# Kernel optimization log

Hardware: AMD Instinct MI355X
Metric: run time of the kernel (lower is better)

Reference implementation:

```python
import jax, jax.numpy as jnp
import numpy as np

B, T, N_IN, UNITS = 256, 1000, 128, 512
TAU, THR, DT = 20.0, 0.01, 1.0
N_REFR = 0
TAU_ADAPT, BETA = 200.0, 1.6
DAMP = 0.3
ADD_CUR = 0.0


def setup_inputs() -> dict:
    key = jax.random.key(0)
    k1, k2, k3 = jax.random.split(key, 3)
    x = jax.random.normal(k1, (B, T, N_IN), jnp.float32)
    # glorot-like scaling so membrane potentials stay in a sane range
    W_in = jax.random.normal(k2, (N_IN, UNITS), jnp.float32) * (1.0 / np.sqrt(N_IN))
    W_rec = jax.random.normal(k3, (UNITS, UNITS), jnp.float32) * (1.0 / np.sqrt(UNITS))
    return {"x": x, "W_in": W_in, "W_rec": W_rec}


@jax.custom_vjp
def spike(v_scaled):
    # Heaviside spike with pseudo-derivative (dampened triangular surrogate)
    return (v_scaled > 0.0).astype(v_scaled.dtype)


def _spike_fwd(v_scaled):
    return (v_scaled > 0.0).astype(v_scaled.dtype), v_scaled


def _spike_bwd(v_scaled, g):
    return (g * DAMP * jnp.maximum(1.0 - jnp.abs(v_scaled), 0.0),)


spike.defvjp(_spike_fwd, _spike_bwd)


def alif_forward(x, W_in, W_rec):
    decay = jnp.exp(-DT / TAU)          # membrane decay
    decay_b = jnp.exp(-DT / TAU_ADAPT)  # adaptation decay
    # recurrent self-connections are disconnected (diagonal zeroed in build)
    W_rec = W_rec * (1.0 - jnp.eye(UNITS, dtype=W_rec.dtype))
    # precompute input currents for all timesteps: [T, B, UNITS]
    i_in_seq = jnp.einsum('bti,iu->tbu', x, W_in)

    def step(state, i_in):
        v, z, b, r = state
        new_b = decay_b * b + (1.0 - decay_b) * z
        thr = THR + new_b * BETA  # adaptive threshold
        i_t = i_in + z @ W_rec + ADD_CUR
        I_reset = z * thr * DT
        new_v = decay * v + (1.0 - decay) * i_t - I_reset
        z_new = spike((new_v - thr) / thr) * (1.0 / DT)
        new_z = jnp.where(r > 0.1, jnp.zeros_like(z_new), z_new)
        new_r = jnp.clip(r + N_REFR * new_z - 1.0, 0.0, float(N_REFR))
        return (new_v, new_z, new_b, new_r), new_z

    zeros = jnp.zeros((B, UNITS), jnp.float32)
    _, zs = jax.lax.scan(step, (zeros, zeros, zeros, zeros), i_in_seq)
    return jnp.transpose(zs, (1, 0, 2))  # [B, T, UNITS]


def reference(x, W_in, W_rec):
    return alif_forward(x, W_in, W_rec)
```

## Files before the change

kernel.cpp:

```cpp
#include <hip/hip_runtime.h>

#define B_SZ   256
#define T_SZ   1000
#define N_IN   128
#define UNITS  512

__global__ __launch_bounds__(512) void wz_prep(const float* __restrict__ Wr,
                                               float* __restrict__ Wz) {
    const int c = threadIdx.x, r = blockIdx.x;
    Wz[(size_t)r * UNITS + c] =
        (r >= UNITS || r == c) ? 0.0f : Wr[(size_t)r * UNITS + c];
}

__global__ __launch_bounds__(256) void gemm_in(const float* __restrict__ X,
                                               const float* __restrict__ W,
                                               float* __restrict__ C) {
    __shared__ __align__(16) float As[32][128];
    __shared__ __align__(16) float Bs[32][128];

    const int tid = threadIdx.x;
    const int ntile = blockIdx.x & 3;
    const int mtile = blockIdx.x >> 2;
    const int m0 = mtile * 128, n0 = ntile * 128;
    const int tm  = (tid >> 4) * 8;
    const int tn4 = (tid & 15) * 4;

    float acc[8][8];
#pragma unroll
    for (int i = 0; i < 8; ++i)
#pragma unroll
        for (int j = 0; j < 8; ++j) acc[i][j] = 0.0f;

    for (int k0 = 0; k0 < 128; k0 += 32) {
        __syncthreads();
#pragma unroll
        for (int r = 0; r < 4; ++r) {
            int li  = r * 256 + tid;
            int row = li >> 3;
            int ch  = li & 7;
            float4 a = *(const float4*)&X[(size_t)(m0 + row) * 128 + k0 + ch * 4];
            As[ch * 4 + 0][row] = a.x;
            As[ch * 4 + 1][row] = a.y;
            As[ch * 4 + 2][row] = a.z;
            As[ch * 4 + 3][row] = a.w;
        }
#pragma unroll
        for (int r = 0; r < 4; ++r) {
            int li = r * 256 + tid;
            int kk = li >> 5;
            int n4 = li & 31;
            *(float4*)&Bs[kk][n4 * 4] =
                *(const float4*)&W[(size_t)(k0 + kk) * 512 + n0 + n4 * 4];
        }
        __syncthreads();

#pragma unroll 8
        for (int k = 0; k < 32; ++k) {
            float4 a0 = *(const float4*)&As[k][tm];
            float4 a1 = *(const float4*)&As[k][tm + 4];
            float4 b0 = *(const float4*)&Bs[k][tn4];
            float4 b1 = *(const float4*)&Bs[k][tn4 + 64];
            const float av[8] = {a0.x, a0.y, a0.z, a0.w, a1.x, a1.y, a1.z, a1.w};
            const float bv[8] = {b0.x, b0.y, b0.z, b0.w, b1.x, b1.y, b1.z, b1.w};
#pragma unroll
            for (int i = 0; i < 8; ++i)
#pragma unroll
                for (int j = 0; j < 8; ++j)
                    acc[i][j] = fmaf(av[i], bv[j], acc[i][j]);
        }
    }

#pragma unroll
    for (int i = 0; i < 8; ++i) {
        size_t row = (size_t)(m0 + tm + i) * 512;
        float4 c0 = make_float4(acc[i][0], acc[i][1], acc[i][2], acc[i][3]);
        float4 c1 = make_float4(acc[i][4], acc[i][5], acc[i][6], acc[i][7]);
        *(float4*)&C[row + n0 + tn4]      = c0;
        *(float4*)&C[row + n0 + 64 + tn4] = c1;
    }
}

__global__ __launch_bounds__(1024, 1) void alif_scan(const float* __restrict__ Wz,
                                                     float* __restrict__ IO) {
    const int tid  = threadIdx.x;
    const int half = tid >> 9;
    const int u    = tid & 511;
    const int w    = u >> 6;
    const int lane = tid & 63;
    const int b    = blockIdx.x * 2 + half;

    __shared__ __align__(16) int s_list[2][520];
    __shared__ int s_cnt[2][8];
    __shared__ int s_total[2];

    const float DECAY   = 0.95122942450071400910f;
    const float OMD     = 1.0f - DECAY;
    const float DECAY_B = 0.99501247919268232342f;
    const float OMDB    = 1.0f - DECAY_B;

    float v = 0.0f, ad = 0.0f, z = 0.0f;

    const float* wz = Wz + u;
    float* io = IO + (size_t)b * (T_SZ * UNITS) + u;
    int* lst = s_list[half];

    lst[u] = UNITS;
    if (u < 8) lst[UNITS + u] = UNITS;
    if (u == 0) s_total[half] = 0;
    __syncthreads();

    float i_cur = io[0];

    for (int t = 0; t < T_SZ; ++t) {
        float i_next = io[(t + 1 < T_SZ ? t + 1 : t) * UNITS];

        const int cnt = s_total[half];
        float acc = 0.0f;

        for (int k = 0; k < cnt; k += 8) {
            int4 Ja = *(const int4*)(lst + k);
            int4 Jb = *(const int4*)(lst + k + 4);
            float g0 = wz[Ja.x * UNITS];
            float g1 = wz[Ja.y * UNITS];
            float g2 = wz[Ja.z * UNITS];
            float g3 = wz[Ja.w * UNITS];
            float g4 = wz[Jb.x * UNITS];
            float g5 = wz[Jb.y * UNITS];
            float g6 = wz[Jb.z * UNITS];
            float g7 = wz[Jb.w * UNITS];
            acc = __fadd_rn(acc, g0);
            acc = __fadd_rn(acc, g1);
            acc = __fadd_rn(acc, g2);
            acc = __fadd_rn(acc, g3);
            acc = __fadd_rn(acc, g4);
            acc = __fadd_rn(acc, g5);
            acc = __fadd_rn(acc, g6);
            acc = __fadd_rn(acc, g7);
        }

        float newb = __fadd_rn(__fmul_rn(DECAY_B, ad), __fmul_rn(OMDB, z));
        float thr  = __fadd_rn(0.01f, __fmul_rn(newb, 1.6f));
        float it   = __fadd_rn(__fadd_rn(i_cur, acc), 0.0f);
        float ires = __fmul_rn(__fmul_rn(z, thr), 1.0f);
        float newv = __fsub_rn(
            __fadd_rn(__fmul_rn(DECAY, v), __fmul_rn(OMD, it)), ires);
        float zn = (newv > thr) ? 1.0f : 0.0f;

        io[t * UNITS] = zn;
        v = newv; ad = newb; z = zn; i_cur = i_next;

        unsigned long long m = __ballot(zn > 0.0f);
        if (lane == 0) s_cnt[half][w] = __popcll(m);
        __syncthreads();

        int base = 0, total = 0;
#pragma unroll
        for (int i = 0; i < 8; ++i) {
            int c = s_cnt[half][i];
            total += c;
            if (i < w) base += c;
        }
        if (zn > 0.0f) {
            int pos = base + __popcll(m & ((1ull << lane) - 1ull));
            lst[pos] = u;
        }
        if (u == 0) s_total[half] = total;
        if (u < 8) lst[total + u] = UNITS;
        __syncthreads();
    }
}

extern "C" void kernel_launch(void* const* d_in, const int* in_sizes, int n_in,
                              void* d_out, int out_size, void* d_ws, size_t ws_size,
                              hipStream_t stream) {
    (void)in_sizes; (void)n_in; (void)out_size; (void)ws_size;
    const float* x     = (const float*)d_in[0];
    const float* W_in  = (const float*)d_in[1];
    const float* W_rec = (const float*)d_in[2];
    float* out = (float*)d_out;
    float* Wz  = (float*)d_ws;

    wz_prep<<<dim3(UNITS + 1), dim3(UNITS), 0, stream>>>(W_rec, Wz);
    gemm_in<<<dim3((B_SZ * T_SZ / 128) * (UNITS / 128)), dim3(256), 0, stream>>>(
        x, W_in, out);
    alif_scan<<<dim3(B_SZ / 2), dim3(1024), 0, stream>>>(Wz, out);
}
```

Measured before the change: 2.206 ms.

## Cache first recurrent weight rows in LDS and run one batch per block

```diff
diff --git a/kernel.cpp b/kernel.cpp
--- a/kernel.cpp
+++ b/kernel.cpp
@@ -4,6 +4,10 @@
 #define T_SZ   1000
 #define N_IN   128
 #define UNITS  512
+#define NC     64
+
+#define SMEM_WORDS (33280 + 528 + 8 + 4)
+#define SMEM_BYTES (SMEM_WORDS * 4)
 
 __global__ __launch_bounds__(512) void wz_prep(const float* __restrict__ Wr,
                                                float* __restrict__ Wz) {
@@ -80,18 +84,18 @@
     }
 }
 
-__global__ __launch_bounds__(1024, 1) void alif_scan(const float* __restrict__ Wz,
-                                                     float* __restrict__ IO) {
-    const int tid  = threadIdx.x;
-    const int half = tid >> 9;
-    const int u    = tid & 511;
-    const int w    = u >> 6;
-    const int lane = tid & 63;
-    const int b    = blockIdx.x * 2 + half;
-
-    __shared__ __align__(16) int s_list[2][520];
-    __shared__ int s_cnt[2][8];
-    __shared__ int s_total[2];
+__global__ __launch_bounds__(512, 2) void alif_scan(const float* __restrict__ Wz,
+                                                    float* __restrict__ IO) {
+    extern __shared__ __align__(16) float smem[];
+    float* lds_w   = smem;
+    int*   lst     = (int*)(smem + (NC + 1) * UNITS);
+    int*   s_cnt   = lst + 528;
+    int*   s_total = s_cnt + 8;
+
+    const int b = blockIdx.x;
+    const int u = threadIdx.x;
+    const int w = u >> 6;
+    const int lane = u & 63;
 
     const float DECAY   = 0.95122942450071400910f;
     const float OMD     = 1.0f - DECAY;
@@ -102,11 +106,14 @@
 
     const float* wz = Wz + u;
     float* io = IO + (size_t)b * (T_SZ * UNITS) + u;
-    int* lst = s_list[half];
-
+
+    for (int idx = u; idx < (NC + 1) * UNITS; idx += 512) {
+        lds_w[idx] = (idx < NC * UNITS) ? Wz[idx] : 0.0f;
+    }
     lst[u] = UNITS;
-    if (u < 8) lst[UNITS + u] = UNITS;
-    if (u == 0) s_total[half] = 0;
+    if (u < 16) lst[UNITS + u] = UNITS;
+    if (u < 8) s_cnt[u] = 0;
+    if (u == 0) *s_total = 0;
     __syncthreads();
 
     float i_cur = io[0];
@@ -114,20 +121,21 @@
     for (int t = 0; t < T_SZ; ++t) {
         float i_next = io[(t + 1 < T_SZ ? t + 1 : t) * UNITS];
 
-        const int cnt = s_total[half];
+        const int cnt = *s_total;
+        const int c0  = s_cnt[0];
         float acc = 0.0f;
 
-        for (int k = 0; k < cnt; k += 8) {
+        for (int k = 0; k < c0; k += 8) {
             int4 Ja = *(const int4*)(lst + k);
             int4 Jb = *(const int4*)(lst + k + 4);
-            float g0 = wz[Ja.x * UNITS];
-            float g1 = wz[Ja.y * UNITS];
-            float g2 = wz[Ja.z * UNITS];
-            float g3 = wz[Ja.w * UNITS];
-            float g4 = wz[Jb.x * UNITS];
-            float g5 = wz[Jb.y * UNITS];
-            float g6 = wz[Jb.z * UNITS];
-            float g7 = wz[Jb.w * UNITS];
+            int j0 = min(Ja.x, NC), j1 = min(Ja.y, NC);
+            int j2 = min(Ja.z, NC), j3 = min(Ja.w, NC);
+            int j4 = min(Jb.x, NC), j5 = min(Jb.y, NC);
+            int j6 = min(Jb.z, NC), j7 = min(Jb.w, NC);
+            float g0 = lds_w[j0 * UNITS + u], g1 = lds_w[j1 * UNITS + u];
+            float g2 = lds_w[j2 * UNITS + u], g3 = lds_w[j3 * UNITS + u];
+            float g4 = lds_w[j4 * UNITS + u], g5 = lds_w[j5 * UNITS + u];
+            float g6 = lds_w[j6 * UNITS + u], g7 = lds_w[j7 * UNITS + u];
             acc = __fadd_rn(acc, g0);
             acc = __fadd_rn(acc, g1);
             acc = __fadd_rn(acc, g2);
@@ -138,6 +146,31 @@
             acc = __fadd_rn(acc, g7);
         }
 
+        for (int k = c0 & ~7; k < cnt; k += 8) {
+            int4 Ja = *(const int4*)(lst + k);
+            int4 Jb = *(const int4*)(lst + k + 4);
+            int j0 = (k + 0 >= c0) ? Ja.x : UNITS;
+            int j1 = (k + 1 >= c0) ? Ja.y : UNITS;
+            int j2 = (k + 2 >= c0) ? Ja.z : UNITS;
+            int j3 = (k + 3 >= c0) ? Ja.w : UNITS;
+            int j4 = (k + 4 >= c0) ? Jb.x : UNITS;
+            int j5 = (k + 5 >= c0) ? Jb.y : UNITS;
+            int j6 = (k + 6 >= c0) ? Jb.z : UNITS;
+            int j7 = (k + 7 >= c0) ? Jb.w : UNITS;
+            float g0 = wz[j0 * UNITS], g1 = wz[j1 * UNITS];
+            float g2 = wz[j2 * UNITS], g3 = wz[j3 * UNITS];
+            float g4 = wz[j4 * UNITS], g5 = wz[j5 * UNITS];
+            float g6 = wz[j6 * UNITS], g7 = wz[j7 * UNITS];
+            acc = __fadd_rn(acc, g0);
+            acc = __fadd_rn(acc, g1);
+            acc = __fadd_rn(acc, g2);
+            acc = __fadd_rn(acc, g3);
+            acc = __fadd_rn(acc, g4);
+            acc = __fadd_rn(acc, g5);
+            acc = __fadd_rn(acc, g6);
+            acc = __fadd_rn(acc, g7);
+        }
+
         float newb = __fadd_rn(__fmul_rn(DECAY_B, ad), __fmul_rn(OMDB, z));
         float thr  = __fadd_rn(0.01f, __fmul_rn(newb, 1.6f));
         float it   = __fadd_rn(__fadd_rn(i_cur, acc), 0.0f);
@@ -150,13 +183,13 @@
         v = newv; ad = newb; z = zn; i_cur = i_next;
 
         unsigned long long m = __ballot(zn > 0.0f);
-        if (lane == 0) s_cnt[half][w] = __popcll(m);
+        if (lane == 0) s_cnt[w] = __popcll(m);
         __syncthreads();
 
         int base = 0, total = 0;
 #pragma unroll
         for (int i = 0; i < 8; ++i) {
-            int c = s_cnt[half][i];
+            int c = s_cnt[i];
             total += c;
             if (i < w) base += c;
         }
@@ -164,8 +197,8 @@
             int pos = base + __popcll(m & ((1ull << lane) - 1ull));
             lst[pos] = u;
         }
-        if (u == 0) s_total[half] = total;
-        if (u < 8) lst[total + u] = UNITS;
+        if (u == 0) *s_total = total;
+        if (u < 16) lst[total + u] = UNITS;
         __syncthreads();
     }
 }
@@ -183,5 +216,8 @@
     wz_prep<<<dim3(UNITS + 1), dim3(UNITS), 0, stream>>>(W_rec, Wz);
     gemm_in<<<dim3((B_SZ * T_SZ / 128) * (UNITS / 128)), dim3(256), 0, stream>>>(
         x, W_in, out);
-    alif_scan<<<dim3(B_SZ / 2), dim3(1024), 0, stream>>>(Wz, out);
-}
+
+    hipFuncSetAttribute((const void*)alif_scan,
+                        hipFuncAttributeMaxDynamicSharedMemorySize, SMEM_BYTES);
+    alif_scan<<<dim3(B_SZ), dim3(512), SMEM_BYTES, stream>>>(Wz, out);
+}
```

Result: faster. 1.999 ms, median of 2 (-9.4%).
